# Kernel tuning notes

Hardware: AMD Instinct MI355X
Metric: run time of the kernel (lower is better)

Reference implementation:

```python
import jax, jax.numpy as jnp
import numpy as np

B, L, D, T = 32, 2048, 64, 512          # batch, seq_len, input_dim, pred steps
H, EK = 2, 64                           # num_heads, embed_dim_per_head
E = H * EK                              # embed_dim = 128
P = 2                                   # function 'L' -> 2 coefficients
LAT, HID = 64, 64                       # latent_dim, hidden_dim
DIM = 2 * D                             # value dim after cat(X, M)


def setup_inputs() -> dict:
    key = jax.random.key(0)
    ks = jax.random.split(key, 20)
    s = 0.05
    inp = {
        "timesteps": jnp.sort(jax.random.uniform(ks[0], (B, L)), axis=-1),
        "X": jax.random.normal(ks[1], (B, L, D)),
        "M": jax.random.bernoulli(ks[2], 0.5, (B, L, D)).astype(jnp.float32),
        "y_time_steps": jnp.sort(jax.random.uniform(ks[3], (B, T)), axis=-1),
        # time_embedding: Linear(1, E)
        "te_w": jax.random.normal(ks[4], (1, E)) * s,
        "te_b": jax.random.normal(ks[5], (E,)) * s,
        # learned queries (1, P, E)
        "query": jax.random.normal(ks[6], (1, P, E)),
        # query_map / key_map: Linear(E, E), stored (in, out)
        "qm_w": jax.random.normal(ks[7], (E, E)) * s,
        "qm_b": jax.random.normal(ks[8], (E,)) * s,
        "km_w": jax.random.normal(ks[9], (E, E)) * s,
        "km_b": jax.random.normal(ks[10], (E,)) * s,
        # shared attention output head: Linear(2*D*H, LAT)
        "out_w": jax.random.normal(ks[11], (DIM * H, LAT)) * s,
        "out_b": jax.random.normal(ks[12], (LAT,)) * s,
        # decoder (depth=1): Linear(LAT, HID) -> ReLU -> Linear(HID, D)
        "dec_w1": jax.random.normal(ks[13], (LAT, HID)) * s,
        "dec_b1": jax.random.normal(ks[14], (HID,)) * s,
        "dec_w2": jax.random.normal(ks[15], (HID, D)) * s,
        "dec_b2": jax.random.normal(ks[16], (D,)) * s,
    }
    return inp


def _forward(timesteps, X, M, y_time_steps, te_w, te_b, query,
             qm_w, qm_b, km_w, km_b, out_w, out_b,
             dec_w1, dec_b1, dec_w2, dec_b2):
    # learn_time_embedding: Linear(1,E) then sin() on indices i % H == 0
    te = timesteps[..., None] @ te_w + te_b                 # (B, L, E)
    sin_idx = (jnp.arange(E) % H) == 0
    key_emb = jnp.where(sin_idx, jnp.sin(te), te)           # (B, L, E)

    value = jnp.concatenate([X, M], axis=-1)                # (B, L, 2D)
    mask = jnp.concatenate([M, M], axis=-1)                 # (B, L, 2D)

    q = query @ qm_w + qm_b                                 # (1, P, E)
    k = key_emb @ km_w + km_b                               # (B, L, E)
    qh = q.reshape(1, P, H, EK).transpose(0, 2, 1, 3)       # (1, H, P, EK)
    kh = k.reshape(B, L, H, EK).transpose(0, 2, 1, 3)       # (B, H, L, EK)

    scores = jnp.einsum('xhpe,bhle->bhpl', qh, kh) / jnp.sqrt(jnp.float32(EK))
    # score broadcast over value dim + per-feature mask fill (-1e9 as in torch)
    logits = jnp.where(mask[:, None, None, :, :] == 0, -1e9,
                       scores[..., None])                   # (B, H, P, L, 2D)
    p_attn = jax.nn.softmax(logits, axis=-2)                # softmax over L
    x = jnp.einsum('bhpld,bld->bhpd', p_attn, value)        # (B, H, P, 2D)

    x = x.transpose(0, 2, 1, 3).reshape(B, P, H * DIM)      # (B, P, H*2D)
    coeffs = x @ out_w + out_b                              # (B, P, LAT)

    # function 'L': linear-in-time latent trajectory
    z = coeffs[:, 0, :][:, None, :] + y_time_steps[..., None] * coeffs[:, 1, :][:, None, :]  # (B, T, LAT)
    h1 = jax.nn.relu(z @ dec_w1 + dec_b1)
    out = h1 @ dec_w2 + dec_b2                              # (B, T, D)
    return out, coeffs


def reference(timesteps, X, M, y_time_steps, te_w, te_b, query,
              qm_w, qm_b, km_w, km_b, out_w, out_b,
              dec_w1, dec_b1, dec_w2, dec_b2):
    return _forward(timesteps, X, M, y_time_steps, te_w, te_b, query,
                    qm_w, qm_b, km_w, km_b, out_w, out_b,
                    dec_w1, dec_b1, dec_w2, dec_b2)
```

## Files before the change

### kernel.cpp

```cpp
#include <hip/hip_runtime.h>
#include <hip/hip_bf16.h>

#define BB 32
#define LL 2048
#define DD 64
#define TT 512
#define INV2PI 0.15915494309189535f

#define NCHUNK 16
#define PSTRIDE 576

__global__ void __launch_bounds__(256) k_attn(
    const float* __restrict__ ts,
    const float* __restrict__ X,
    const float* __restrict__ M,
    const float* __restrict__ te_w,
    const float* __restrict__ te_b,
    const float* __restrict__ query,
    const float* __restrict__ qm_w,
    const float* __restrict__ qm_b,
    const float* __restrict__ km_w,
    const float* __restrict__ km_b,
    float* __restrict__ ws) {
  __shared__ float q_lds[256];
  __shared__ float r_lds[512];
  __shared__ __align__(16) float rp4[256];
  __shared__ __align__(8)  float feat2[128];
  __shared__ float tsl[128];
  __shared__ float C0[4], C1[4];
  __shared__ float sred[1024];
  __shared__ float w_lds[512];
  __shared__ float red[256 * 18];
  const int t = threadIdx.x;
  const int b = blockIdx.y;
  const int lc = blockIdx.x * 128;

  if (t < 128) tsl[t] = ts[(size_t)b * LL + lc + t];
  if (t < 64) {
    feat2[2 * t]     = te_w[2 * t] * INV2PI;
    feat2[2 * t + 1] = te_b[2 * t] * INV2PI;
  }

  {
    const int p = t >> 7, e = t & 127;
    const float* qq = query + p * 128;
    const float* qw = qm_w + e;
    float a0 = 0.f, a1 = 0.f, a2 = 0.f, a3 = 0.f;
    for (int i = 0; i < 128; i += 4) {
      a0 += qq[i]     * qw[i * 128];
      a1 += qq[i + 1] * qw[(i + 1) * 128];
      a2 += qq[i + 2] * qw[(i + 2) * 128];
      a3 += qq[i + 3] * qw[(i + 3) * 128];
    }
    q_lds[t] = (a0 + a1) + (a2 + a3) + qm_b[e];
  }

  const int dpair = t & 31, lr = t >> 5;
  const float2* X2 = (const float2*)X;
  const float2* M2 = (const float2*)M;
  const size_t base = ((size_t)b * LL + lc) * 32;
  float2 xa[8], ma[8];
#pragma unroll
  for (int i = 0; i < 8; ++i) {
    xa[i] = X2[base + (size_t)(lr + i * 8) * 32 + dpair];
    ma[i] = M2[base + (size_t)(lr + i * 8) * 32 + dpair];
  }
  __syncthreads();

  for (int o = t; o < 512; o += 256) {
    const int hp = o >> 7, i = o & 127;
    const int h = hp >> 1, p = hp & 1;
    const float4* km4 = (const float4*)(km_w + i * 128 + h * 64);
    const float* qp = &q_lds[p * 128 + h * 64];
    float acc = 0.f;
#pragma unroll
    for (int e4 = 0; e4 < 16; ++e4) {
      const float4 w = km4[e4];
      acc += qp[4 * e4] * w.x + qp[4 * e4 + 1] * w.y +
             qp[4 * e4 + 2] * w.z + qp[4 * e4 + 3] * w.w;
    }
    r_lds[o] = acc;
  }
  __syncthreads();

  if (t < 64) {
#pragma unroll
    for (int hp = 0; hp < 4; ++hp) rp4[t * 4 + hp] = r_lds[hp * 128 + 2 * t];
  }
  if (t >= 64 && t < 72) {
    const int hp = (t - 64) >> 1;
    if ((t & 1) == 0) {
      float s = 0.f;
      for (int e = 0; e < 64; ++e) s += te_w[2 * e + 1] * r_lds[hp * 128 + 2 * e + 1];
      C1[hp] = s;
    } else {
      float s = 0.f;
      for (int e = 0; e < 64; ++e) s += te_b[2 * e + 1] * r_lds[hp * 128 + 2 * e + 1];
      const int h = hp >> 1, p = hp & 1;
      float c = 0.f;
      for (int e = 0; e < 64; ++e) c += q_lds[p * 128 + h * 64 + e] * km_b[h * 64 + e];
      C0[hp] = s + c;
    }
  }
  __syncthreads();

  {
    const int l = t >> 1, half = t & 1;
    const float tt = tsl[l];
    const float2* f2 = (const float2*)feat2;
    const float4* r4 = (const float4*)rp4;
    float p0 = 0.f, p1 = 0.f, p2 = 0.f, p3 = 0.f;
    const int e0 = half * 32;
    for (int e = e0; e < e0 + 32; ++e) {
      const float2 wb = f2[e];
      const float f = __builtin_amdgcn_sinf(tt * wb.x + wb.y);
      const float4 r = r4[e];
      p0 += f * r.x; p1 += f * r.y; p2 += f * r.z; p3 += f * r.w;
    }
    sred[t * 4 + 0] = p0; sred[t * 4 + 1] = p1;
    sred[t * 4 + 2] = p2; sred[t * 4 + 3] = p3;
  }
  __syncthreads();
  {
    const int l = t >> 1, pr = t & 1;
    const float tt = tsl[l];
#pragma unroll
    for (int k2 = 0; k2 < 2; ++k2) {
      const int hp = pr * 2 + k2;
      const float s = sred[(2 * l) * 4 + hp] + sred[(2 * l + 1) * 4 + hp] +
                      tt * C1[hp] + C0[hp];
      w_lds[l * 4 + hp] = __expf(s * 0.125f);
    }
  }
  __syncthreads();

  float n[4][2] = {}, dn[4][2] = {}, sx[2] = {};
#pragma unroll
  for (int i = 0; i < 8; ++i) {
    const int ll = lr + i * 8;
    const float2 xv = xa[i], mv = ma[i];
    const float mx0 = mv.x * xv.x, mx1 = mv.y * xv.y;
    sx[0] += xv.x; sx[1] += xv.y;
#pragma unroll
    for (int hp = 0; hp < 4; ++hp) {
      const float w = w_lds[ll * 4 + hp];
      n[hp][0]  += w * mx0;  n[hp][1]  += w * mx1;
      dn[hp][0] += w * mv.x; dn[hp][1] += w * mv.y;
    }
  }
  for (int i = 8; i < 16; ++i) {
    const int ll = lr + i * 8;
    const float2 xv = X2[base + (size_t)ll * 32 + dpair];
    const float2 mv = M2[base + (size_t)ll * 32 + dpair];
    const float mx0 = mv.x * xv.x, mx1 = mv.y * xv.y;
    sx[0] += xv.x; sx[1] += xv.y;
#pragma unroll
    for (int hp = 0; hp < 4; ++hp) {
      const float w = w_lds[ll * 4 + hp];
      n[hp][0]  += w * mx0;  n[hp][1]  += w * mx1;
      dn[hp][0] += w * mv.x; dn[hp][1] += w * mv.y;
    }
  }

#pragma unroll
  for (int hp = 0; hp < 4; ++hp) {
    red[t * 18 + hp * 2 + 0] = n[hp][0];
    red[t * 18 + hp * 2 + 1] = n[hp][1];
    red[t * 18 + 8 + hp * 2 + 0] = dn[hp][0];
    red[t * 18 + 8 + hp * 2 + 1] = dn[hp][1];
  }
  red[t * 18 + 16] = sx[0];
  red[t * 18 + 17] = sx[1];
  __syncthreads();

  if (t < 32) {
    float* slot = ws + ((size_t)b * NCHUNK + blockIdx.x) * PSTRIDE;
    for (int j = 0; j < 18; ++j) {
      float s = 0.f;
#pragma unroll
      for (int r2 = 0; r2 < 8; ++r2) s += red[(r2 * 32 + t) * 18 + j];
      if (j < 8) {
        const int hp = j >> 1, half = j & 1;
        slot[hp * 64 + 2 * t + half] = s;
      } else if (j < 16) {
        const int j2 = j - 8, hp = j2 >> 1, half = j2 & 1;
        slot[256 + hp * 64 + 2 * t + half] = s;
      } else {
        slot[512 + 2 * t + (j - 16)] = s;
      }
    }
  }
}

__global__ void __launch_bounds__(256) k_dec(
    const float* __restrict__ yts,
    const float* __restrict__ out_w,
    const float* __restrict__ out_b,
    const float* __restrict__ dec_w1,
    const float* __restrict__ dec_b1,
    const float* __restrict__ dec_w2,
    const float* __restrict__ dec_b2,
    const float* __restrict__ ws,
    float* __restrict__ out) {
  __shared__ __align__(16) float acc_l[576];
  __shared__ float x_lds[512];
  __shared__ float cred[256];
  __shared__ float c_lds[128];
  __shared__ float abred[256];
  __shared__ float ABl[128];
  __shared__ __align__(16) float w2l[4096];
  __shared__ float h1l[1024];
  __shared__ float b2l[64], yl[64];
  const int t = threadIdx.x;
  const int b = blockIdx.y;
  const int t0 = blockIdx.x * 64;

  {
    const float4* s4 = (const float4*)dec_w2;
    float4* d4 = (float4*)w2l;
    for (int i = t; i < 1024; i += 256) d4[i] = s4[i];
  }
  if (t < 144) {
    const float4* p4 = (const float4*)(ws + (size_t)b * NCHUNK * PSTRIDE);
    float4 s; s.x = s.y = s.z = s.w = 0.f;
    for (int c = 0; c < NCHUNK; ++c) {
      const float4 v = p4[(size_t)c * 144 + t];
      s.x += v.x; s.y += v.y; s.z += v.z; s.w += v.w;
    }
    ((float4*)acc_l)[t] = s;
  }
  if (t >= 192) {
    const int k = t - 192;
    b2l[k] = dec_b2[k];
    yl[k] = yts[b * TT + t0 + k];
  }
  __syncthreads();

  {
    const int hp = t >> 6, d = t & 63;
    const int h = hp >> 1, p = hp & 1;
    const float num = acc_l[hp * 64 + d];
    const float den = acc_l[256 + hp * 64 + d];
    const float sxv = acc_l[512 + d];
    float x1, x2;
    if (den > 0.f) { x1 = num / den; x2 = 1.f; }
    else           { x1 = sxv * (1.f / (float)LL); x2 = 0.f; }
    x_lds[p * 256 + h * 128 + d] = x1;
    x_lds[p * 256 + h * 128 + 64 + d] = x2;
  }
  __syncthreads();

  {
    const int kh = t >> 7, pj = t & 127, p = pj >> 6, j = pj & 63;
    float acc = (kh == 0) ? out_b[j] : 0.f;
    const float* xp = &x_lds[p * 256 + kh * 128];
    const float* wp = out_w + (size_t)kh * 128 * 64 + j;
    for (int k = 0; k < 128; ++k) acc += xp[k] * wp[k * 64];
    cred[t] = acc;
  }
  __syncthreads();
  if (t < 128) {
    const float c = cred[t] + cred[t + 128];
    c_lds[t] = c;
    if (blockIdx.x == 0)
      out[(size_t)BB * TT * DD + b * 128 + t] = c;
  }
  __syncthreads();
  if (t < 128) {
    const int jh = t >> 6, k = t & 63;
    float a = 0.f, bb = 0.f;
    const float* cp = &c_lds[jh * 32];
    const float* cp2 = &c_lds[64 + jh * 32];
    for (int j = 0; j < 32; ++j) {
      const float w1 = dec_w1[(jh * 32 + j) * 64 + k];
      a += cp[j] * w1;
      bb += cp2[j] * w1;
    }
    abred[t * 2] = a;
    abred[t * 2 + 1] = bb;
  }
  __syncthreads();
  if (t < 64) {
    ABl[t]      = dec_b1[t] + abred[t * 2]     + abred[(64 + t) * 2];
    ABl[64 + t] =             abred[t * 2 + 1] + abred[(64 + t) * 2 + 1];
  }
  __syncthreads();

  const int tl = t >> 4, dg = t & 15;
  for (int it = 0; it < 4; ++it) {
    {
      int idx = t;
#pragma unroll
      for (int rr = 0; rr < 4; ++rr, idx += 256) {
        const int tl2 = idx >> 6, k = idx & 63;
        h1l[idx] = fmaxf(ABl[k] + yl[it * 16 + tl2] * ABl[64 + k], 0.f);
      }
    }
    __syncthreads();
    {
      float a0 = b2l[dg * 4], a1 = b2l[dg * 4 + 1],
            a2 = b2l[dg * 4 + 2], a3 = b2l[dg * 4 + 3];
      const float4* w4 = (const float4*)w2l;
      const float* h1p = &h1l[tl * 64];
      for (int k = 0; k < 64; ++k) {
        const float h = h1p[k];
        const float4 w = w4[k * 16 + dg];
        a0 += h * w.x; a1 += h * w.y; a2 += h * w.z; a3 += h * w.w;
      }
      const int tg = t0 + it * 16 + tl;
      const size_t off = ((size_t)b * TT + tg) * 64 + dg * 4;
      float4 o; o.x = a0; o.y = a1; o.z = a2; o.w = a3;
      *(float4*)(out + off) = o;
    }
    __syncthreads();
  }
}

extern "C" void kernel_launch(void* const* d_in, const int* in_sizes, int n_in,
                              void* d_out, int out_size, void* d_ws, size_t ws_size,
                              hipStream_t stream) {
  const float* ts     = (const float*)d_in[0];
  const float* X      = (const float*)d_in[1];
  const float* M      = (const float*)d_in[2];
  const float* yts    = (const float*)d_in[3];
  const float* te_w   = (const float*)d_in[4];
  const float* te_b   = (const float*)d_in[5];
  const float* query  = (const float*)d_in[6];
  const float* qm_w   = (const float*)d_in[7];
  const float* qm_b   = (const float*)d_in[8];
  const float* km_w   = (const float*)d_in[9];
  const float* km_b   = (const float*)d_in[10];
  const float* out_w  = (const float*)d_in[11];
  const float* out_b  = (const float*)d_in[12];
  const float* dec_w1 = (const float*)d_in[13];
  const float* dec_b1 = (const float*)d_in[14];
  const float* dec_w2 = (const float*)d_in[15];
  const float* dec_b2 = (const float*)d_in[16];
  float* ws = (float*)d_ws;
  float* out = (float*)d_out;

  k_attn<<<dim3(NCHUNK, BB), 256, 0, stream>>>(
      ts, X, M, te_w, te_b, query, qm_w, qm_b, km_w, km_b, ws);
  k_dec<<<dim3(TT / 64, BB), 256, 0, stream>>>(
      yts, out_w, out_b, dec_w1, dec_b1, dec_w2, dec_b2, ws, out);
}
```

Baseline: 133.3 us.

## Vectorize X/M loads to float4, parallelize chunk reduction, stage params in LDS

Each thread now owns four adjacent features and eight rows. X and M are loaded as float4 in a single prefetch batch, replacing the float2 loads split between a prefetch and an in-loop fetch. Attention weights are read once per row as a float4 from LDS. The final cross-thread reduction spreads across 144 threads that each write one float4 slot, replacing 32 threads looping serially over 18 outputs. te_w, te_b and km_b are staged in LDS so the scalar constant loops avoid global loads. The cost is a doubled LDS reduction buffer and more live registers, which may lower occupancy.

```diff
diff --git a/kernel.cpp b/kernel.cpp
--- a/kernel.cpp
+++ b/kernel.cpp
@@ -22,23 +22,24 @@
     const float* __restrict__ km_w,
     const float* __restrict__ km_b,
     float* __restrict__ ws) {
+  __shared__ float tsl[128], tew[128], teb[128], kmb[128];
   __shared__ float q_lds[256];
   __shared__ float r_lds[512];
   __shared__ __align__(16) float rp4[256];
   __shared__ __align__(8)  float feat2[128];
-  __shared__ float tsl[128];
   __shared__ float C0[4], C1[4];
   __shared__ float sred[1024];
-  __shared__ float w_lds[512];
-  __shared__ float red[256 * 18];
+  __shared__ __align__(16) float w_lds[512];
+  __shared__ float red[256 * 36];
   const int t = threadIdx.x;
   const int b = blockIdx.y;
   const int lc = blockIdx.x * 128;
 
-  if (t < 128) tsl[t] = ts[(size_t)b * LL + lc + t];
-  if (t < 64) {
-    feat2[2 * t]     = te_w[2 * t] * INV2PI;
-    feat2[2 * t + 1] = te_b[2 * t] * INV2PI;
+  if (t < 128) {
+    tsl[t] = ts[(size_t)b * LL + lc + t];
+    tew[t] = te_w[t];
+    teb[t] = te_b[t];
+    kmb[t] = km_b[t];
   }
 
   {
@@ -54,19 +55,12 @@
     }
     q_lds[t] = (a0 + a1) + (a2 + a3) + qm_b[e];
   }
-
-  const int dpair = t & 31, lr = t >> 5;
-  const float2* X2 = (const float2*)X;
-  const float2* M2 = (const float2*)M;
-  const size_t base = ((size_t)b * LL + lc) * 32;
-  float2 xa[8], ma[8];
-#pragma unroll
-  for (int i = 0; i < 8; ++i) {
-    xa[i] = X2[base + (size_t)(lr + i * 8) * 32 + dpair];
-    ma[i] = M2[base + (size_t)(lr + i * 8) * 32 + dpair];
-  }
-  __syncthreads();
-
+  __syncthreads();
+
+  if (t < 64) {
+    feat2[2 * t]     = tew[2 * t] * INV2PI;
+    feat2[2 * t + 1] = teb[2 * t] * INV2PI;
+  }
   for (int o = t; o < 512; o += 256) {
     const int hp = o >> 7, i = o & 127;
     const int h = hp >> 1, p = hp & 1;
@@ -83,6 +77,17 @@
   }
   __syncthreads();
 
+  const int dquad = t & 15, lr = t >> 4;
+  const float4* X4 = (const float4*)X;
+  const float4* M4 = (const float4*)M;
+  const size_t base4 = ((size_t)b * LL + lc) * 16;
+  float4 xa[8], ma[8];
+#pragma unroll
+  for (int i = 0; i < 8; ++i) {
+    xa[i] = X4[base4 + (size_t)(lr + i * 16) * 16 + dquad];
+    ma[i] = M4[base4 + (size_t)(lr + i * 16) * 16 + dquad];
+  }
+
   if (t < 64) {
 #pragma unroll
     for (int hp = 0; hp < 4; ++hp) rp4[t * 4 + hp] = r_lds[hp * 128 + 2 * t];
@@ -91,14 +96,14 @@
     const int hp = (t - 64) >> 1;
     if ((t & 1) == 0) {
       float s = 0.f;
-      for (int e = 0; e < 64; ++e) s += te_w[2 * e + 1] * r_lds[hp * 128 + 2 * e + 1];
+      for (int e = 0; e < 64; ++e) s += tew[2 * e + 1] * r_lds[hp * 128 + 2 * e + 1];
       C1[hp] = s;
     } else {
       float s = 0.f;
-      for (int e = 0; e < 64; ++e) s += te_b[2 * e + 1] * r_lds[hp * 128 + 2 * e + 1];
+      for (int e = 0; e < 64; ++e) s += teb[2 * e + 1] * r_lds[hp * 128 + 2 * e + 1];
       const int h = hp >> 1, p = hp & 1;
       float c = 0.f;
-      for (int e = 0; e < 64; ++e) c += q_lds[p * 128 + h * 64 + e] * km_b[h * 64 + e];
+      for (int e = 0; e < 64; ++e) c += q_lds[p * 128 + h * 64 + e] * kmb[h * 64 + e];
       C0[hp] = s + c;
     }
   }
@@ -134,61 +139,51 @@
   }
   __syncthreads();
 
-  float n[4][2] = {}, dn[4][2] = {}, sx[2] = {};
+  float n[4][4] = {}, dn[4][4] = {}, sx[4] = {};
+  const float4* wl4 = (const float4*)w_lds;
 #pragma unroll
   for (int i = 0; i < 8; ++i) {
-    const int ll = lr + i * 8;
-    const float2 xv = xa[i], mv = ma[i];
-    const float mx0 = mv.x * xv.x, mx1 = mv.y * xv.y;
-    sx[0] += xv.x; sx[1] += xv.y;
-#pragma unroll
-    for (int hp = 0; hp < 4; ++hp) {
-      const float w = w_lds[ll * 4 + hp];
-      n[hp][0]  += w * mx0;  n[hp][1]  += w * mx1;
-      dn[hp][0] += w * mv.x; dn[hp][1] += w * mv.y;
-    }
-  }
-  for (int i = 8; i < 16; ++i) {
-    const int ll = lr + i * 8;
-    const float2 xv = X2[base + (size_t)ll * 32 + dpair];
-    const float2 mv = M2[base + (size_t)ll * 32 + dpair];
-    const float mx0 = mv.x * xv.x, mx1 = mv.y * xv.y;
-    sx[0] += xv.x; sx[1] += xv.y;
-#pragma unroll
-    for (int hp = 0; hp < 4; ++hp) {
-      const float w = w_lds[ll * 4 + hp];
-      n[hp][0]  += w * mx0;  n[hp][1]  += w * mx1;
-      dn[hp][0] += w * mv.x; dn[hp][1] += w * mv.y;
-    }
-  }
-
-#pragma unroll
-  for (int hp = 0; hp < 4; ++hp) {
-    red[t * 18 + hp * 2 + 0] = n[hp][0];
-    red[t * 18 + hp * 2 + 1] = n[hp][1];
-    red[t * 18 + 8 + hp * 2 + 0] = dn[hp][0];
-    red[t * 18 + 8 + hp * 2 + 1] = dn[hp][1];
-  }
-  red[t * 18 + 16] = sx[0];
-  red[t * 18 + 17] = sx[1];
-  __syncthreads();
-
-  if (t < 32) {
-    float* slot = ws + ((size_t)b * NCHUNK + blockIdx.x) * PSTRIDE;
-    for (int j = 0; j < 18; ++j) {
-      float s = 0.f;
-#pragma unroll
-      for (int r2 = 0; r2 < 8; ++r2) s += red[(r2 * 32 + t) * 18 + j];
-      if (j < 8) {
-        const int hp = j >> 1, half = j & 1;
-        slot[hp * 64 + 2 * t + half] = s;
-      } else if (j < 16) {
-        const int j2 = j - 8, hp = j2 >> 1, half = j2 & 1;
-        slot[256 + hp * 64 + 2 * t + half] = s;
-      } else {
-        slot[512 + 2 * t + (j - 16)] = s;
-      }
-    }
+    const int ll = lr + i * 16;
+    const float4 xv = xa[i], mv = ma[i];
+    const float4 wv = wl4[ll];
+    const float mx0 = mv.x * xv.x, mx1 = mv.y * xv.y,
+                mx2 = mv.z * xv.z, mx3 = mv.w * xv.w;
+    sx[0] += xv.x; sx[1] += xv.y; sx[2] += xv.z; sx[3] += xv.w;
+    const float w0 = wv.x, w1 = wv.y, w2 = wv.z, w3 = wv.w;
+    n[0][0] += w0 * mx0; n[0][1] += w0 * mx1; n[0][2] += w0 * mx2; n[0][3] += w0 * mx3;
+    n[1][0] += w1 * mx0; n[1][1] += w1 * mx1; n[1][2] += w1 * mx2; n[1][3] += w1 * mx3;
+    n[2][0] += w2 * mx0; n[2][1] += w2 * mx1; n[2][2] += w2 * mx2; n[2][3] += w2 * mx3;
+    n[3][0] += w3 * mx0; n[3][1] += w3 * mx1; n[3][2] += w3 * mx2; n[3][3] += w3 * mx3;
+    dn[0][0] += w0 * mv.x; dn[0][1] += w0 * mv.y; dn[0][2] += w0 * mv.z; dn[0][3] += w0 * mv.w;
+    dn[1][0] += w1 * mv.x; dn[1][1] += w1 * mv.y; dn[1][2] += w1 * mv.z; dn[1][3] += w1 * mv.w;
+    dn[2][0] += w2 * mv.x; dn[2][1] += w2 * mv.y; dn[2][2] += w2 * mv.z; dn[2][3] += w2 * mv.w;
+    dn[3][0] += w3 * mv.x; dn[3][1] += w3 * mv.y; dn[3][2] += w3 * mv.z; dn[3][3] += w3 * mv.w;
+  }
+
+  {
+    float* rp = &red[t * 36];
+#pragma unroll
+    for (int hp = 0; hp < 4; ++hp)
+#pragma unroll
+      for (int k = 0; k < 4; ++k) { rp[hp * 4 + k] = n[hp][k]; rp[16 + hp * 4 + k] = dn[hp][k]; }
+#pragma unroll
+    for (int k = 0; k < 4; ++k) rp[32 + k] = sx[k];
+  }
+  __syncthreads();
+
+  if (t < 144) {
+    int dq, j0;
+    if (t < 64)        { dq = t & 15;         j0 = (t >> 4) * 4; }
+    else if (t < 128)  { dq = (t - 64) & 15;  j0 = 16 + ((t - 64) >> 4) * 4; }
+    else               { dq = t - 128;        j0 = 32; }
+    float4 s; s.x = s.y = s.z = s.w = 0.f;
+#pragma unroll
+    for (int g = 0; g < 16; ++g) {
+      const float* rp = &red[(g * 16 + dq) * 36 + j0];
+      s.x += rp[0]; s.y += rp[1]; s.z += rp[2]; s.w += rp[3];
+    }
+    float4* slot4 = (float4*)(ws + ((size_t)b * NCHUNK + blockIdx.x) * PSTRIDE);
+    slot4[t] = s;
   }
 }
 
```

Result: slower. 137.5 us (+3.2%).
